# Kernel optimization log

Measured on AMD Instinct MI355X. Metric: run time of the kernel, lower is better.

The kernel has to match this reference:

```python
import jax, jax.numpy as jnp
import numpy as np
import math

DIM = 512
HEADS = 8
DIM_HEAD = 64
SCALE = math.sqrt(DIM_HEAD)
EPS = 1e-12


def rms_norm(x, g):
    # F.normalize(x, dim=1) * g * sqrt(dim); x: [B, C, H, W], g: [C]
    inv = jax.lax.rsqrt(jnp.sum(x * x, axis=1, keepdims=True) + EPS)
    return x * inv * g[None, :, None, None] * jnp.asarray(math.sqrt(x.shape[1]), x.dtype)


def setup_inputs() -> dict:
    key = jax.random.key(0)
    k1, k2, k3 = jax.random.split(key, 3)
    B, H, W = 8, 64, 64
    hidden = HEADS * DIM_HEAD
    x = jax.random.normal(k1, (B, DIM, H, W), dtype=jnp.float32)
    w_qkv = jax.random.normal(k2, (3 * hidden, DIM), dtype=jnp.float32) * (1.0 / math.sqrt(DIM))
    w_out = jax.random.normal(k3, (DIM, hidden), dtype=jnp.float32) * (1.0 / math.sqrt(hidden))
    b_out = jnp.zeros((DIM,), dtype=jnp.float32)
    g1 = jnp.ones((DIM,), dtype=jnp.float32)
    g2 = jnp.ones((DIM,), dtype=jnp.float32)
    return {"x": x, "g1": g1, "w_qkv": w_qkv, "w_out": w_out, "b_out": b_out, "g2": g2}


def reference(x, g1, w_qkv, w_out, b_out, g2):
    B, C, H, W = x.shape
    n = H * W
    xn = rms_norm(x, g1)
    # 1x1 conv == channel matmul: [B, 3*hidden, H, W]
    qkv = jnp.einsum('bchw,oc->bohw', xn, w_qkv)
    q, k, v = jnp.split(qkv, 3, axis=1)
    # b (h c) x y -> b h c n
    def to_heads(t):
        return t.reshape(B, HEADS, DIM_HEAD, n)
    q, k, v = to_heads(q), to_heads(k), to_heads(v)
    q = jax.nn.softmax(q, axis=2) / SCALE   # softmax over channel dim d
    k = jax.nn.softmax(k, axis=3)           # softmax over spatial dim n
    context = jnp.einsum('bhdn,bhen->bhde', k, v)   # [B, H, d, e]
    out = jnp.einsum('bhde,bhdn->bhen', context, q) # [B, H, e, n]
    out = out.reshape(B, HEADS * DIM_HEAD, H, W)
    out = jnp.einsum('bchw,oc->bohw', out, w_out) + b_out[None, :, None, None]
    return rms_norm(out, g2)
```

## Files before the change

### kernel.cpp

```cpp
#include <hip/hip_runtime.h>


typedef unsigned short u16;
typedef __attribute__((ext_vector_type(8))) short short8;
typedef __attribute__((ext_vector_type(4))) short short4_t;
typedef __attribute__((ext_vector_type(4))) float f32x4;

static constexpr size_t XN_B = (size_t)512 * 4096;
static constexpr size_t KV_B = (size_t)1024 * 4096;
static constexpr float SQRT512 = 22.62741699796952f;

typedef const __attribute__((address_space(1))) unsigned int gu32;
typedef __attribute__((address_space(3))) unsigned int lu32;

__device__ __forceinline__ float b2f(u16 u){
  union { unsigned u; float f; } x; x.u = ((unsigned)u) << 16; return x.f;
}
__device__ __forceinline__ u16 f2b(float f){
  union { float f; unsigned u; } x; x.f = f;
  unsigned r = x.u + 0x7FFFu + ((x.u >> 16) & 1u);
  return (u16)(r >> 16);
}
__device__ __forceinline__ void gl16(const u16* g, u16* l){
  __builtin_amdgcn_global_load_lds((gu32*)g, (lu32*)l, 16, 0, 0);
}

__global__ __launch_bounds__(256)
void kprep(const float* __restrict__ wqkv, const float* __restrict__ wout,
           const float* __restrict__ g1, u16* __restrict__ dq, u16* __restrict__ dw,
           const float* __restrict__ x, u16* __restrict__ xnT){
  __shared__ u16 lt[32][514];
  __shared__ float red[256];
  __shared__ float invs[32];
  int bid = blockIdx.x;
  int t = threadIdx.x;
  if (bid < 1024){
    size_t i = ((size_t)bid * 256 + t) * 4;
    short4_t o;
    if (i < (size_t)786432){
      f32x4 v = *(const f32x4*)(wqkv + i);
      int c = (int)(i & 511);
      #pragma unroll
      for (int j = 0; j < 4; j++) o[j] = (short)f2b(v[j] * g1[c + j] * SQRT512);
      *(short4_t*)(dq + i) = o;
    } else {
      size_t off = i - 786432;
      f32x4 v = *(const f32x4*)(wout + off);
      #pragma unroll
      for (int j = 0; j < 4; j++) o[j] = (short)f2b(v[j]);
      *(short4_t*)(dw + off) = o;
    }
    return;
  }
  int pg0 = (bid - 1024) * 32;
  int b = pg0 >> 12, p0 = pg0 & 4095;
  int px = t & 31, chunk = t >> 5;
  const float* xp = x + (size_t)b * XN_B + p0 + px;
  float s = 0.f;
  #pragma unroll 4
  for (int c = chunk * 64; c < chunk * 64 + 64; ++c){
    float v = xp[(size_t)c * 4096];
    lt[px][c] = f2b(v);
    s += v * v;
  }
  red[t] = s;
  __syncthreads();
  if (chunk == 0){
    float tt = red[px] + red[px + 32] + red[px + 64] + red[px + 96]
             + red[px + 128] + red[px + 160] + red[px + 192] + red[px + 224];
    invs[px] = rsqrtf(tt + 1e-12f);
  }
  __syncthreads();
  int px2 = t >> 3, c0 = (t & 7) * 8;
  float iv = invs[px2];
  u16* dst = xnT + (size_t)(pg0 + px2) * 512;
  #pragma unroll
  for (int j = 0; j < 8; j++){
    int c = c0 + j * 64;
    short8 o;
    #pragma unroll
    for (int e = 0; e < 8; e++) o[e] = (short)f2b(b2f(lt[px2][c + e]) * iv);
    *(short8*)(dst + c) = o;
  }
}

template<int ADD_BIAS, int SMAX>
__global__ __launch_bounds__(512)
void gemm_big(const u16* __restrict__ Ab, long astr, int lda,
              const u16* __restrict__ Bb, long bstr, int ldb,
              u16* __restrict__ Cb, long cstr, int ldc,
              const float* __restrict__ bias)
{
  constexpr int NT = 16;
  const u16* A  = Ab + (size_t)blockIdx.z * astr;
  const u16* BT = Bb + (size_t)blockIdx.z * bstr;
  u16* C = Cb + (size_t)blockIdx.z * cstr;
  const int m0 = blockIdx.y * 256, n0 = blockIdx.x * 256;
  __shared__ u16 As[2][256 * 32];
  __shared__ u16 Bs[2][256 * 32];
  const int tid = threadIdx.x;
  const int lane = tid & 63, wid = tid >> 6;
  const int wr = (wid >> 2) * 128, wc = (wid & 3) * 64;
  const int fr = lane & 15, fq = lane >> 4;
  const int srow = tid >> 2;
  const int sslot = tid & 3;
  f32x4 acc[8][4] = {};

  auto STAGE = [&](int s, int t){
    const int k0 = t * 32;
    #pragma unroll
    for (int r = 0; r < 2; r++){
      int row = r * 128 + srow;
      int gj = (sslot ^ ((row >> 1) & 3)) * 8;
      gl16(A  + (size_t)(m0 + row) * lda + k0 + gj, &As[s][0] + r * 4096 + tid * 8);
      gl16(BT + (size_t)(n0 + row) * ldb + k0 + gj, &Bs[s][0] + r * 4096 + tid * 8);
    }
  };

  STAGE(0, 0);
  int cur = 0;
  for (int t = 0; t < NT; t++){
    if (t + 1 < NT){
      STAGE(cur ^ 1, t + 1);
      asm volatile("s_waitcnt vmcnt(4)" ::: "memory");
    } else {
      asm volatile("s_waitcnt vmcnt(0)" ::: "memory");
    }
    __builtin_amdgcn_s_barrier();
    __builtin_amdgcn_sched_barrier(0);
    short8 a[8], b[4];
    #pragma unroll
    for (int i = 0; i < 8; i++){
      int ra = wr + i * 16 + fr;
      a[i] = *(const short8*)(&As[cur][0] + ra * 32 + ((fq ^ ((ra >> 1) & 3)) * 8));
    }
    #pragma unroll
    for (int j = 0; j < 4; j++){
      int rb = wc + j * 16 + fr;
      b[j] = *(const short8*)(&Bs[cur][0] + rb * 32 + ((fq ^ ((rb >> 1) & 3)) * 8));
    }
    __builtin_amdgcn_s_setprio(1);
    #pragma unroll
    for (int i = 0; i < 8; i++)
      #pragma unroll
      for (int j = 0; j < 4; j++)
        acc[i][j] = __builtin_amdgcn_mfma_f32_16x16x32_bf16(a[i], b[j], acc[i][j], 0, 0, 0);
    __builtin_amdgcn_s_setprio(0);
    __builtin_amdgcn_sched_barrier(0);
    __builtin_amdgcn_s_barrier();
    cur ^= 1;
  }

  if constexpr (SMAX){
    #pragma unroll
    for (int i = 0; i < 8; i++)
      #pragma unroll
      for (int e = 0; e < 4; e++){
        float mx = fmaxf(fmaxf(acc[i][0][e], acc[i][1][e]),
                         fmaxf(acc[i][2][e], acc[i][3][e]));
        mx = fmaxf(mx, __shfl_xor(mx, 1));
        mx = fmaxf(mx, __shfl_xor(mx, 2));
        mx = fmaxf(mx, __shfl_xor(mx, 4));
        mx = fmaxf(mx, __shfl_xor(mx, 8));
        float p0 = __expf(acc[i][0][e] - mx);
        float p1 = __expf(acc[i][1][e] - mx);
        float p2 = __expf(acc[i][2][e] - mx);
        float p3 = __expf(acc[i][3][e] - mx);
        float s = p0 + p1 + p2 + p3;
        s += __shfl_xor(s, 1);
        s += __shfl_xor(s, 2);
        s += __shfl_xor(s, 4);
        s += __shfl_xor(s, 8);
        float r = 1.f / (s * 8.0f);
        acc[i][0][e] = p0 * r; acc[i][1][e] = p1 * r;
        acc[i][2][e] = p2 * r; acc[i][3][e] = p3 * r;
      }
  }
  #pragma unroll
  for (int i = 0; i < 8; i++)
    #pragma unroll
    for (int j = 0; j < 4; j++)
      #pragma unroll
      for (int e = 0; e < 4; e++){
        int row = m0 + wr + i * 16 + fq * 4 + e;
        int col = n0 + wc + j * 16 + fr;
        float v = acc[i][j][e];
        if constexpr (ADD_BIAS) v += bias[col];
        C[(size_t)row * ldc + col] = f2b(v);
      }
}

__global__ __launch_bounds__(256)
void gemm_kv(const u16* __restrict__ Wkv, const u16* __restrict__ xnT,
             u16* __restrict__ kvb)
{
  constexpr int NT = 8;
  const int z = blockIdx.z;
  const u16* A  = Wkv;
  const u16* BT = xnT + (size_t)z * XN_B;
  u16* C = kvb + (size_t)z * KV_B;
  const int m0 = blockIdx.y * 128, n0 = blockIdx.x * 128;
  __shared__ u16 As[2][128 * 64];
  __shared__ u16 Bs[2][128 * 64];
  const int tid = threadIdx.x;
  const int srow0 = tid >> 3;
  const int schunk = tid & 7;
  const int lane = tid & 63, wid = tid >> 6;
  const int wr = (wid >> 1) * 64, wc = (wid & 1) * 64;
  const int fr = lane & 15, fq = lane >> 4;
  f32x4 acc[4][4] = {};

  auto STAGE = [&](int s, int t){
    const int k0 = t * 64;
    #pragma unroll
    for (int r = 0; r < 4; r++){
      int row = r * 32 + srow0;
      int gj = (schunk ^ (row & 7)) * 8;
      gl16(A  + (size_t)(m0 + row) * 512 + k0 + gj, &As[s][0] + r * 2048 + tid * 8);
      gl16(BT + (size_t)(n0 + row) * 512 + k0 + gj, &Bs[s][0] + r * 2048 + tid * 8);
    }
  };

  STAGE(0, 0);
  int cur = 0;
  for (int t = 0; t < NT; t++){
    if (t + 1 < NT){
      STAGE(cur ^ 1, t + 1);
      asm volatile("s_waitcnt vmcnt(8)" ::: "memory");
    } else {
      asm volatile("s_waitcnt vmcnt(0)" ::: "memory");
    }
    __builtin_amdgcn_s_barrier();
    __builtin_amdgcn_sched_barrier(0);
    #pragma unroll
    for (int ks = 0; ks < 2; ks++){
      short8 a[4], b[4];
      #pragma unroll
      for (int i = 0; i < 4; i++){
        int ra = wr + i * 16 + fr;
        a[i] = *(const short8*)(&As[cur][0] + ra * 64 + ((ks * 4 + fq) ^ (ra & 7)) * 8);
        int rb = wc + i * 16 + fr;
        b[i] = *(const short8*)(&Bs[cur][0] + rb * 64 + ((ks * 4 + fq) ^ (rb & 7)) * 8);
      }
      #pragma unroll
      for (int i = 0; i < 4; i++)
        #pragma unroll
        for (int j = 0; j < 4; j++)
          acc[i][j] = __builtin_amdgcn_mfma_f32_16x16x32_bf16(a[i], b[j], acc[i][j], 0, 0, 0);
    }
    __builtin_amdgcn_sched_barrier(0);
    __builtin_amdgcn_s_barrier();
    cur ^= 1;
  }

  #pragma unroll
  for (int i = 0; i < 4; i++)
    #pragma unroll
    for (int j = 0; j < 4; j++)
      #pragma unroll
      for (int e = 0; e < 4; e++){
        int row = m0 + wr + i * 16 + fq * 4 + e;
        int col = n0 + wc + j * 16 + fr;
        C[(size_t)row * 4096 + col] = f2b(acc[i][j][e]);
      }
}

__global__ __launch_bounds__(256)
void kstats(const u16* __restrict__ kv, float* __restrict__ stats){
  int bx = blockIdx.x;
  int b = bx >> 9, c = bx & 511;
  const u16* kp = kv + (size_t)b * KV_B + (size_t)c * 4096;
  int tid = threadIdx.x;
  float s = 0.f;
  #pragma unroll
  for (int j = 0; j < 2; j++){
    short8 t = *(const short8*)(kp + j * 2048 + tid * 8);
    #pragma unroll
    for (int e = 0; e < 8; e++) s += __expf(b2f((u16)t[e]));
  }
  #pragma unroll
  for (int o = 32; o >= 1; o >>= 1) s += __shfl_xor(s, o);
  __shared__ float reds[4];
  if ((tid & 63) == 0) reds[tid >> 6] = s;
  __syncthreads();
  if (tid == 0)
    stats[bx] = 1.f / (reds[0] + reds[1] + reds[2] + reds[3]);
}

__global__ __launch_bounds__(256)
void gemm_ctx(const u16* __restrict__ kv, float* __restrict__ P,
              const float* __restrict__ stats)
{
  constexpr int K = 512;
  const int z = blockIdx.z;
  const int tid = threadIdx.x;
  const int ar = tid >> 2, ac = (tid & 3) * 8;
  int bh = z >> 3, sp = z & 7, b = bh >> 3, h = bh & 7;
  const u16* A  = kv + (size_t)b * KV_B + (size_t)(h * 64) * 4096 + sp * 512;
  const u16* BT = kv + (size_t)b * KV_B + (size_t)(512 + h * 64) * 4096 + sp * 512;
  float rsr = stats[b * 512 + h * 64 + ar];
  __shared__ u16 As[64 * 40];
  __shared__ u16 Bs[64 * 40];
  const int wid = tid >> 6, lane = tid & 63;
  const int wr = (wid >> 1) * 32, wc = (wid & 1) * 32;
  const int lr = lane & 15, kb = lane >> 4;
  f32x4 acc[2][2] = {};
  for (int k0 = 0; k0 < K; k0 += 32){
    short8 av = *(const short8*)(A + (size_t)ar * 4096 + k0 + ac);
    short8 ao;
    #pragma unroll
    for (int e = 0; e < 8; e++)
      ao[e] = (short)f2b(__expf(b2f((u16)av[e])) * rsr);
    *(short8*)(As + ar * 40 + ac) = ao;
    *(short8*)(Bs + ar * 40 + ac) = *(const short8*)(BT + (size_t)ar * 4096 + k0 + ac);
    __syncthreads();
    short8 a0 = *(const short8*)(As + (wr +      lr) * 40 + kb * 8);
    short8 a1 = *(const short8*)(As + (wr + 16 + lr) * 40 + kb * 8);
    short8 b0 = *(const short8*)(Bs + (wc +      lr) * 40 + kb * 8);
    short8 b1 = *(const short8*)(Bs + (wc + 16 + lr) * 40 + kb * 8);
    acc[0][0] = __builtin_amdgcn_mfma_f32_16x16x32_bf16(a0, b0, acc[0][0], 0, 0, 0);
    acc[0][1] = __builtin_amdgcn_mfma_f32_16x16x32_bf16(a0, b1, acc[0][1], 0, 0, 0);
    acc[1][0] = __builtin_amdgcn_mfma_f32_16x16x32_bf16(a1, b0, acc[1][0], 0, 0, 0);
    acc[1][1] = __builtin_amdgcn_mfma_f32_16x16x32_bf16(a1, b1, acc[1][1], 0, 0, 0);
    __syncthreads();
  }
  #pragma unroll
  for (int mi = 0; mi < 2; mi++)
    #pragma unroll
    for (int ni = 0; ni < 2; ni++)
      #pragma unroll
      for (int j = 0; j < 4; j++){
        int row = wr + mi * 16 + kb * 4 + j;
        int col = wc + ni * 16 + lr;
        P[(size_t)z * 4096 + (size_t)row * 64 + col] = acc[mi][ni][j];
      }
}

__global__ __launch_bounds__(256)
void kctxw(const float* __restrict__ P, const u16* __restrict__ woutbf,
           u16* __restrict__ M)
{
  const int z = blockIdx.z;
  const int b = z >> 3, h = z & 7;
  const int m0 = blockIdx.y * 64;
  const int tid = threadIdx.x;
  __shared__ u16 As[64 * 72];
  __shared__ u16 Bs[64 * 72];
  {
    int r = tid >> 2, c0 = (tid & 3) * 16;
    const u16* wsrc = woutbf + (size_t)(m0 + r) * 512 + h * 64 + c0;
    *(short8*)(As + r * 72 + c0)     = *(const short8*)(wsrc);
    *(short8*)(As + r * 72 + c0 + 8) = *(const short8*)(wsrc + 8);
    const float* p = P + (size_t)z * 32768 + (size_t)r * 64 + c0;
    #pragma unroll
    for (int e = 0; e < 16; e++){
      float s = 0.f;
      #pragma unroll
      for (int sp = 0; sp < 8; sp++) s += p[e + sp * 4096];
      Bs[r * 72 + c0 + e] = f2b(s);
    }
  }
  __syncthreads();
  const int wid = tid >> 6, lane = tid & 63;
  const int wr = (wid >> 1) * 32, wc = (wid & 1) * 32;
  const int lr = lane & 15, kb = lane >> 4;
  f32x4 acc[2][2] = {};
  #pragma unroll
  for (int k0 = 0; k0 < 64; k0 += 32){
    short8 a0 = *(const short8*)(As + (wr +      lr) * 72 + k0 + kb * 8);
    short8 a1 = *(const short8*)(As + (wr + 16 + lr) * 72 + k0 + kb * 8);
    short8 b0 = *(const short8*)(Bs + (wc +      lr) * 72 + k0 + kb * 8);
    short8 b1 = *(const short8*)(Bs + (wc + 16 + lr) * 72 + k0 + kb * 8);
    acc[0][0] = __builtin_amdgcn_mfma_f32_16x16x32_bf16(a0, b0, acc[0][0], 0, 0, 0);
    acc[0][1] = __builtin_amdgcn_mfma_f32_16x16x32_bf16(a0, b1, acc[0][1], 0, 0, 0);
    acc[1][0] = __builtin_amdgcn_mfma_f32_16x16x32_bf16(a1, b0, acc[1][0], 0, 0, 0);
    acc[1][1] = __builtin_amdgcn_mfma_f32_16x16x32_bf16(a1, b1, acc[1][1], 0, 0, 0);
  }
  #pragma unroll
  for (int mi = 0; mi < 2; mi++)
    #pragma unroll
    for (int ni = 0; ni < 2; ni++)
      #pragma unroll
      for (int j = 0; j < 4; j++){
        int row = m0 + wr + mi * 16 + kb * 4 + j;
        int col = wc + ni * 16 + lr;
        M[(size_t)b * 262144 + (size_t)row * 512 + h * 64 + col] = f2b(acc[mi][ni][j]);
      }
}

__global__ __launch_bounds__(256)
void krms2(const u16* __restrict__ o2, const float* __restrict__ g,
           float* __restrict__ out){
  __shared__ u16 lt[32][514];
  __shared__ float invs[32];
  __shared__ float gl[512];
  int t = threadIdx.x;
  int pg0 = blockIdx.x * 32;
  int b = pg0 >> 12, p0 = pg0 & 4095;
  gl[t] = g[t] * SQRT512;
  gl[t + 256] = g[t + 256] * SQRT512;
  int px2 = t >> 3, c0 = (t & 7) * 8;
  const u16* src = o2 + (size_t)(pg0 + px2) * 512;
  float s = 0.f;
  #pragma unroll
  for (int j = 0; j < 8; j++){
    int c = c0 + j * 64;
    short8 v = *(const short8*)(src + c);
    *(short8*)&lt[px2][c] = v;
    #pragma unroll
    for (int e = 0; e < 8; e++){ float f = b2f((u16)v[e]); s += f * f; }
  }
  s += __shfl_xor(s, 1); s += __shfl_xor(s, 2); s += __shfl_xor(s, 4);
  if ((t & 7) == 0) invs[px2] = rsqrtf(s + 1e-12f);
  __syncthreads();
  int c2 = t >> 2, pxc = (t & 3) * 8;
  float ivv[8];
  #pragma unroll
  for (int e = 0; e < 8; e++) ivv[e] = invs[pxc + e];
  #pragma unroll
  for (int pass = 0; pass < 8; pass++){
    int c = c2 + pass * 64;
    float gf = gl[c];
    float* dst = out + ((size_t)(b * 512 + c)) * 4096 + p0 + pxc;
    #pragma unroll
    for (int q = 0; q < 2; q++){
      f32x4 o;
      #pragma unroll
      for (int e = 0; e < 4; e++){
        int pp = q * 4 + e;
        o[e] = b2f(lt[pxc + pp][c]) * ivv[pp] * gf;
      }
      *(f32x4*)(dst + q * 4) = o;
    }
  }
}

extern "C" void kernel_launch(void* const* d_in, const int* in_sizes, int n_in,
                              void* d_out, int out_size, void* d_ws, size_t ws_size,
                              hipStream_t stream)
{
  (void)in_sizes; (void)n_in; (void)out_size; (void)ws_size;
  const float* x    = (const float*)d_in[0];
  const float* g1   = (const float*)d_in[1];
  const float* wqkv = (const float*)d_in[2];
  const float* wout = (const float*)d_in[3];
  const float* bout = (const float*)d_in[4];
  const float* g2   = (const float*)d_in[5];
  float* out = (float*)d_out;
  char* ws = (char*)d_ws;

  u16*   xnT   = (u16*)(ws);
  float* P     = (float*)(ws);
  u16*   M     = (u16*)(ws + (size_t)8388608);
  u16*   qT    = (u16*)(ws + (size_t)33554432);
  u16*   kv    = (u16*)(ws + (size_t)67108864);
  u16*   out2T = (u16*)(ws + (size_t)67108864);
  u16*   wbf   = (u16*)(ws + (size_t)134217728);
  u16*   wkvbf = wbf + (size_t)512 * 512;
  u16*   woutbf= (u16*)(ws + (size_t)135790592);
  float* stats = (float*)(ws + (size_t)136314880);

  kprep<<<2048, 256, 0, stream>>>(wqkv, wout, g1, wbf, woutbf, x, xnT);
  gemm_big<0, 1><<<dim3(2, 128, 1), 512, 0, stream>>>(xnT, 0, 512, wbf, 0, 512,
                                                      qT, 0, 512, nullptr);
  gemm_kv<<<dim3(32, 8, 8), 256, 0, stream>>>(wkvbf, xnT, kv);
  kstats<<<4096, 256, 0, stream>>>(kv, stats);
  gemm_ctx<<<dim3(1, 1, 512), 256, 0, stream>>>(kv, P, stats);
  kctxw<<<dim3(1, 8, 64), 256, 0, stream>>>(P, woutbf, M);
  gemm_big<1, 0><<<dim3(2, 16, 8), 512, 0, stream>>>(qT, (long)4096 * 512, 512,
                                                     M, (long)262144, 512,
                                                     out2T, (long)4096 * 512, 512, bout);
  krms2<<<1024, 256, 0, stream>>>(out2T, g2, out);
}
```

Baseline: 191.0 us.

## Fuse k softmax denominator into context GEMM via atomics, drop stats kernel

Removes the separate kstats pass over the K half of kv. gemm_ctx now accumulates the exp-sum per row while it computes exp(k) and adds partial sums to a buffer with atomicAdd; kprep zeroes that buffer first. kctxw then applies the normalisation by scaling the summed context rows. This saves one kernel launch and one full read of K, in exchange for atomics and bf16 rounding of the unnormalised exp values.

```diff
diff --git a/kernel.cpp b/kernel.cpp
--- a/kernel.cpp
+++ b/kernel.cpp
@@ -28,13 +28,15 @@
 __global__ __launch_bounds__(256)
 void kprep(const float* __restrict__ wqkv, const float* __restrict__ wout,
            const float* __restrict__ g1, u16* __restrict__ dq, u16* __restrict__ dw,
-           const float* __restrict__ x, u16* __restrict__ xnT){
+           const float* __restrict__ x, u16* __restrict__ xnT,
+           float* __restrict__ sden){
   __shared__ u16 lt[32][514];
   __shared__ float red[256];
   __shared__ float invs[32];
   int bid = blockIdx.x;
   int t = threadIdx.x;
   if (bid < 1024){
+    if (bid < 16) sden[bid * 256 + t] = 0.f;
     size_t i = ((size_t)bid * 256 + t) * 4;
     short4_t o;
     if (i < (size_t)786432){
@@ -266,30 +268,8 @@
 }
 
 __global__ __launch_bounds__(256)
-void kstats(const u16* __restrict__ kv, float* __restrict__ stats){
-  int bx = blockIdx.x;
-  int b = bx >> 9, c = bx & 511;
-  const u16* kp = kv + (size_t)b * KV_B + (size_t)c * 4096;
-  int tid = threadIdx.x;
-  float s = 0.f;
-  #pragma unroll
-  for (int j = 0; j < 2; j++){
-    short8 t = *(const short8*)(kp + j * 2048 + tid * 8);
-    #pragma unroll
-    for (int e = 0; e < 8; e++) s += __expf(b2f((u16)t[e]));
-  }
-  #pragma unroll
-  for (int o = 32; o >= 1; o >>= 1) s += __shfl_xor(s, o);
-  __shared__ float reds[4];
-  if ((tid & 63) == 0) reds[tid >> 6] = s;
-  __syncthreads();
-  if (tid == 0)
-    stats[bx] = 1.f / (reds[0] + reds[1] + reds[2] + reds[3]);
-}
-
-__global__ __launch_bounds__(256)
 void gemm_ctx(const u16* __restrict__ kv, float* __restrict__ P,
-              const float* __restrict__ stats)
+              float* __restrict__ sden)
 {
   constexpr int K = 512;
   const int z = blockIdx.z;
@@ -298,19 +278,22 @@
   int bh = z >> 3, sp = z & 7, b = bh >> 3, h = bh & 7;
   const u16* A  = kv + (size_t)b * KV_B + (size_t)(h * 64) * 4096 + sp * 512;
   const u16* BT = kv + (size_t)b * KV_B + (size_t)(512 + h * 64) * 4096 + sp * 512;
-  float rsr = stats[b * 512 + h * 64 + ar];
   __shared__ u16 As[64 * 40];
   __shared__ u16 Bs[64 * 40];
   const int wid = tid >> 6, lane = tid & 63;
   const int wr = (wid >> 1) * 32, wc = (wid & 1) * 32;
   const int lr = lane & 15, kb = lane >> 4;
   f32x4 acc[2][2] = {};
+  float ssum = 0.f;
   for (int k0 = 0; k0 < K; k0 += 32){
     short8 av = *(const short8*)(A + (size_t)ar * 4096 + k0 + ac);
     short8 ao;
     #pragma unroll
-    for (int e = 0; e < 8; e++)
-      ao[e] = (short)f2b(__expf(b2f((u16)av[e])) * rsr);
+    for (int e = 0; e < 8; e++){
+      float ev = __expf(b2f((u16)av[e]));
+      ao[e] = (short)f2b(ev);
+      ssum += ev;
+    }
     *(short8*)(As + ar * 40 + ac) = ao;
     *(short8*)(Bs + ar * 40 + ac) = *(const short8*)(BT + (size_t)ar * 4096 + k0 + ac);
     __syncthreads();
@@ -324,6 +307,9 @@
     acc[1][1] = __builtin_amdgcn_mfma_f32_16x16x32_bf16(a1, b1, acc[1][1], 0, 0, 0);
     __syncthreads();
   }
+  ssum += __shfl_xor(ssum, 1);
+  ssum += __shfl_xor(ssum, 2);
+  if ((tid & 3) == 0) atomicAdd(sden + b * 512 + h * 64 + ar, ssum);
   #pragma unroll
   for (int mi = 0; mi < 2; mi++)
     #pragma unroll
@@ -337,8 +323,8 @@
 }
 
 __global__ __launch_bounds__(256)
-void kctxw(const float* __restrict__ P, const u16* __restrict__ woutbf,
-           u16* __restrict__ M)
+void kctxw(const float* __restrict__ P, const float* __restrict__ sden,
+           const u16* __restrict__ woutbf, u16* __restrict__ M)
 {
   const int z = blockIdx.z;
   const int b = z >> 3, h = z & 7;
@@ -351,13 +337,14 @@
     const u16* wsrc = woutbf + (size_t)(m0 + r) * 512 + h * 64 + c0;
     *(short8*)(As + r * 72 + c0)     = *(const short8*)(wsrc);
     *(short8*)(As + r * 72 + c0 + 8) = *(const short8*)(wsrc + 8);
+    float rs = 1.f / sden[b * 512 + h * 64 + r];
     const float* p = P + (size_t)z * 32768 + (size_t)r * 64 + c0;
     #pragma unroll
     for (int e = 0; e < 16; e++){
       float s = 0.f;
       #pragma unroll
       for (int sp = 0; sp < 8; sp++) s += p[e + sp * 4096];
-      Bs[r * 72 + c0 + e] = f2b(s);
+      Bs[r * 72 + c0 + e] = f2b(s * rs);
     }
   }
   __syncthreads();
@@ -458,15 +445,14 @@
   u16*   wbf   = (u16*)(ws + (size_t)134217728);
   u16*   wkvbf = wbf + (size_t)512 * 512;
   u16*   woutbf= (u16*)(ws + (size_t)135790592);
-  float* stats = (float*)(ws + (size_t)136314880);
-
-  kprep<<<2048, 256, 0, stream>>>(wqkv, wout, g1, wbf, woutbf, x, xnT);
+  float* sden  = (float*)(ws + (size_t)136314880);
+
+  kprep<<<2048, 256, 0, stream>>>(wqkv, wout, g1, wbf, woutbf, x, xnT, sden);
   gemm_big<0, 1><<<dim3(2, 128, 1), 512, 0, stream>>>(xnT, 0, 512, wbf, 0, 512,
                                                       qT, 0, 512, nullptr);
   gemm_kv<<<dim3(32, 8, 8), 256, 0, stream>>>(wkvbf, xnT, kv);
-  kstats<<<4096, 256, 0, stream>>>(kv, stats);
-  gemm_ctx<<<dim3(1, 1, 512), 256, 0, stream>>>(kv, P, stats);
-  kctxw<<<dim3(1, 8, 64), 256, 0, stream>>>(P, woutbf, M);
+  gemm_ctx<<<dim3(1, 1, 512), 256, 0, stream>>>(kv, P, sden);
+  kctxw<<<dim3(1, 8, 64), 256, 0, stream>>>(P, sden, woutbf, M);
   gemm_big<1, 0><<<dim3(2, 16, 8), 512, 0, stream>>>(qT, (long)4096 * 512, 512,
                                                      M, (long)262144, 512,
                                                      out2T, (long)4096 * 512, 512, bout);
```

Result: faster. 184.3 us (-3.5%).
